# Optimization experiments

Hardware: AMD Instinct MI355X
Metric: run time of the kernel (lower is better)

The kernel has to match this reference:

```python
import jax, jax.numpy as jnp
import numpy as np


def setup_inputs() -> dict:
    key = jax.random.key(0)
    k1, k2, k3 = jax.random.split(key, 3)
    seq_len, input_size, hidden_size = 8192, 2048, 2048
    inputs = jax.random.normal(k1, (seq_len, input_size), dtype=jnp.float32)
    W_xh = jax.random.normal(k2, (hidden_size, input_size), dtype=jnp.float32) * 0.01
    W_hh = jax.random.normal(k3, (hidden_size, hidden_size), dtype=jnp.float32) * 0.01
    b_h = jnp.zeros((hidden_size, 1), dtype=jnp.float32)
    return {"inputs": inputs, "W_xh": W_xh, "W_hh": W_hh, "b_h": b_h}


def reference(inputs, W_xh, W_hh, b_h):
    # h_t = tanh(W_xh @ x_t + W_hh @ h_{t-1} + b_h), h_0 = 0
    # Torch code uses column vectors (hidden,1); we use flat (hidden,) vectors,
    # which is the same math.
    b = b_h[:, 0]
    h0 = jnp.zeros((W_hh.shape[0],), dtype=inputs.dtype)

    def step(h_prev, x_t):
        h_t = jnp.tanh(W_xh @ x_t + W_hh @ h_prev + b)
        return h_t, h_t

    h_T, outputs = jax.lax.scan(step, h0, inputs)
    # outputs: (seq_len, hidden)  == stacked list of h_t; h_T == final state
    return outputs, h_T
```

## Files before the change

### kernel.cpp

```cpp
#include <hip/hip_runtime.h>
#include <math.h>

#define H 2048
#define S 8192
#define RPB 16
#define NBLK (H / RPB)
#define PARBYTES (H * 4)
#define NREP 2

typedef unsigned int u32x4 __attribute__((ext_vector_type(4)));

__global__ __launch_bounds__(256) void gemm_xw(const float* __restrict__ X,
                                               const float* __restrict__ W,
                                               float* __restrict__ U) {
    __shared__ float As[16][64];
    __shared__ float Bs[16][64];
    const int tid = threadIdx.x;
    const int t0 = blockIdx.x * 64;
    const int j0 = blockIdx.y * 64;
    const int tx = tid & 15, ty = tid >> 4;

    float acc[4][4] = {};
    const int lr = tid >> 2;
    const int lk = (tid & 3) * 4;

    for (int k0 = 0; k0 < H; k0 += 16) {
        float4 a = *(const float4*)&X[(size_t)(t0 + lr) * H + k0 + lk];
        float4 b = *(const float4*)&W[(size_t)(j0 + lr) * H + k0 + lk];
        As[lk + 0][lr] = a.x; As[lk + 1][lr] = a.y; As[lk + 2][lr] = a.z; As[lk + 3][lr] = a.w;
        Bs[lk + 0][lr] = b.x; Bs[lk + 1][lr] = b.y; Bs[lk + 2][lr] = b.z; Bs[lk + 3][lr] = b.w;
        __syncthreads();
#pragma unroll
        for (int kk = 0; kk < 16; ++kk) {
            float4 av = *(const float4*)&As[kk][ty * 4];
            float4 bv = *(const float4*)&Bs[kk][tx * 4];
            float aa[4] = {av.x, av.y, av.z, av.w};
            float bb[4] = {bv.x, bv.y, bv.z, bv.w};
#pragma unroll
            for (int i = 0; i < 4; ++i)
#pragma unroll
                for (int j = 0; j < 4; ++j)
                    acc[i][j] += aa[i] * bb[j];
        }
        __syncthreads();
    }
#pragma unroll
    for (int i = 0; i < 4; ++i) {
        float4 v = {acc[i][0], acc[i][1], acc[i][2], acc[i][3]};
        *(float4*)&U[(size_t)(t0 + ty * 4 + i) * H + j0 + tx * 4] = v;
    }
}

__global__ void init_ws(unsigned long long* __restrict__ w) {
    int i = blockIdx.x * blockDim.x + threadIdx.x;
    if (i < NREP * 2 * (PARBYTES / 8))
        w[i] = ((i >> 10) & 1) ? 0x0000000100000001ull : 0ull;
}

__device__ inline void poll2(const void* pc, u32x4& c0, u32x4& c1) {
    asm volatile(
        "global_load_dwordx4 %0, %2, off sc1\n\t"
        "global_load_dwordx4 %1, %2, off offset:16 sc1\n\t"
        "s_waitcnt vmcnt(0)"
        : "=&v"(c0), "=&v"(c1)
        : "v"(pc)
        : "memory");
}
__device__ inline void st16_sc1(void* p, u32x4 v) {
    asm volatile("global_store_dwordx4 %0, %1, off sc1" :: "v"(p), "v"(v) : "memory");
}

__global__ __launch_bounds__(256) void rnn_recur(float* __restrict__ out,
                                                 const float* __restrict__ Whh,
                                                 const float* __restrict__ bias,
                                                 unsigned long long* __restrict__ hvt) {
    __shared__ float part[2][4][RPB];
    const int tid  = threadIdx.x;
    const int lane = tid & 63;
    const int wid  = tid >> 6;
    const int r0   = blockIdx.x * RPB;

    float4 wv[RPB][2];
#pragma unroll
    for (int j = 0; j < RPB; ++j)
#pragma unroll
        for (int i = 0; i < 2; ++i)
            wv[j][i] = *(const float4*)&Whh[(size_t)(r0 + j) * H + 8 * tid + 4 * i];

    const float bb = bias[r0 + (tid & 15)];
    char* const hrep = (char*)hvt + (size_t)(blockIdx.x & 1) * (2 * PARBYTES);

    for (int t = 0; t < S; ++t) {
        float u_val = out[(size_t)t * H + r0 + (tid & 15)];

        const unsigned int e  = ((unsigned int)t >> 1) & 3u;
        const unsigned int e0 = e & 1u, e1 = (e >> 1) & 1u;
        const char* pc = hrep + (size_t)(t & 1) * PARBYTES + tid * 32;

        float acc[RPB] = {};
        unsigned int pend = 3u;
        while (pend) {
            u32x4 c0, c1;
            poll2(pc, c0, c1);
#pragma unroll
            for (int i = 0; i < 2; ++i) {
                if (pend & (1u << i)) {
                    const u32x4 v = i ? c1 : c0;
                    if ((((v.x ^ e0) | (v.z ^ e0) | (v.y ^ e1) | (v.w ^ e1)) & 1u) == 0u) {
                        const float h0 = __uint_as_float(v.x), h1 = __uint_as_float(v.y);
                        const float h2 = __uint_as_float(v.z), h3 = __uint_as_float(v.w);
#pragma unroll
                        for (int j = 0; j < RPB; ++j)
                            acc[j] += wv[j][i].x * h0 + wv[j][i].y * h1 +
                                      wv[j][i].z * h2 + wv[j][i].w * h3;
                        pend &= ~(1u << i);
                    }
                }
            }
        }

#pragma unroll
        for (int j = 0; j < 8; ++j) {
            float s = (lane & 1) ? acc[j] : acc[j + 8];
            float r = __shfl_xor(s, 1, 64);
            acc[j] = ((lane & 1) ? acc[j + 8] : acc[j]) + r;
        }
#pragma unroll
        for (int j = 0; j < 4; ++j) {
            float s = (lane & 2) ? acc[j] : acc[j + 4];
            float r = __shfl_xor(s, 2, 64);
            acc[j] = ((lane & 2) ? acc[j + 4] : acc[j]) + r;
        }
#pragma unroll
        for (int j = 0; j < 2; ++j) {
            float s = (lane & 4) ? acc[j] : acc[j + 2];
            float r = __shfl_xor(s, 4, 64);
            acc[j] = ((lane & 4) ? acc[j + 2] : acc[j]) + r;
        }
        {
            float s = (lane & 8) ? acc[0] : acc[1];
            float r = __shfl_xor(s, 8, 64);
            acc[0] = ((lane & 8) ? acc[1] : acc[0]) + r;
        }
        acc[0] += __shfl_xor(acc[0], 16, 64);
        acc[0] += __shfl_xor(acc[0], 32, 64);

        if (lane < 16) {
            const int row = ((lane & 1) << 3) | ((lane & 2) << 1) |
                            ((lane & 4) >> 1) | ((lane & 8) >> 3);
            part[t & 1][wid][row] = acc[0];
        }
        __syncthreads();

        if (tid < RPB) {
            const float sum = part[t & 1][0][tid] + part[t & 1][1][tid] +
                              part[t & 1][2][tid] + part[t & 1][3][tid];
            const float val = tanhf(sum + u_val + bb);
            const float s0 = __shfl(val, (tid & 12) | 0, 64);
            const float s1 = __shfl(val, (tid & 12) | 1, 64);
            const float s2 = __shfl(val, (tid & 12) | 2, 64);
            const float s3 = __shfl(val, (tid & 12) | 3, 64);
            if ((tid & 3) == 0) {
                const unsigned int ee  = (((unsigned int)(t + 1)) >> 1) & 3u;
                const unsigned int ee0 = ee & 1u, ee1 = (ee >> 1) & 1u;
                u32x4 pk;
                pk.x = (__float_as_uint(s0) & ~1u) | ee0;
                pk.y = (__float_as_uint(s1) & ~1u) | ee1;
                pk.z = (__float_as_uint(s2) & ~1u) | ee0;
                pk.w = (__float_as_uint(s3) & ~1u) | ee1;
                char* dst = (char*)hvt + (size_t)((t + 1) & 1) * PARBYTES +
                            (size_t)(r0 + tid) * 4;
                asm volatile("s_waitcnt vmcnt(0)" ::: "memory");
#pragma unroll
                for (int rep = 0; rep < NREP; ++rep)
                    st16_sc1(dst + (size_t)rep * (2 * PARBYTES), pk);
            }
            out[(size_t)t * H + r0 + tid] = val;
            if (t == S - 1) out[(size_t)S * H + r0 + tid] = val;
        }
    }
}

extern "C" void kernel_launch(void* const* d_in, const int* in_sizes, int n_in,
                              void* d_out, int out_size, void* d_ws, size_t ws_size,
                              hipStream_t stream) {
    const float* X    = (const float*)d_in[0];
    const float* Wxh  = (const float*)d_in[1];
    const float* Whh  = (const float*)d_in[2];
    const float* bias = (const float*)d_in[3];
    float* out = (float*)d_out;
    unsigned long long* hvt = (unsigned long long*)d_ws;

    init_ws<<<(NREP * 2 * (PARBYTES / 8) + 255) / 256, 256, 0, stream>>>(hvt);

    dim3 ggrid(S / 64, H / 64);
    gemm_xw<<<ggrid, 256, 0, stream>>>(X, Wxh, out);

    void* args[] = {(void*)&out, (void*)&Whh, (void*)&bias, (void*)&hvt};
    hipLaunchCooperativeKernel((void*)rnn_recur, dim3(NBLK), dim3(256), args, 0, stream);
}
```

Before: 19.65 ms.

## Rebalance recurrent kernel to 64 blocks of 512 threads with 32 rows each

```diff
diff --git a/kernel.cpp b/kernel.cpp
--- a/kernel.cpp
+++ b/kernel.cpp
@@ -3,8 +3,9 @@
 
 #define H 2048
 #define S 8192
-#define RPB 16
+#define RPB 32
 #define NBLK (H / RPB)
+#define TPB 512
 #define PARBYTES (H * 4)
 #define NREP 2
 
@@ -57,109 +58,107 @@
         w[i] = ((i >> 10) & 1) ? 0x0000000100000001ull : 0ull;
 }
 
-__device__ inline void poll2(const void* pc, u32x4& c0, u32x4& c1) {
-    asm volatile(
-        "global_load_dwordx4 %0, %2, off sc1\n\t"
-        "global_load_dwordx4 %1, %2, off offset:16 sc1\n\t"
-        "s_waitcnt vmcnt(0)"
-        : "=&v"(c0), "=&v"(c1)
-        : "v"(pc)
-        : "memory");
+__device__ inline u32x4 ld16_sc1(const void* p) {
+    u32x4 r;
+    asm volatile("global_load_dwordx4 %0, %1, off sc1\n\t"
+                 "s_waitcnt vmcnt(0)"
+                 : "=&v"(r) : "v"(p) : "memory");
+    return r;
 }
 __device__ inline void st16_sc1(void* p, u32x4 v) {
     asm volatile("global_store_dwordx4 %0, %1, off sc1" :: "v"(p), "v"(v) : "memory");
 }
 
-__global__ __launch_bounds__(256) void rnn_recur(float* __restrict__ out,
-                                                 const float* __restrict__ Whh,
-                                                 const float* __restrict__ bias,
-                                                 unsigned long long* __restrict__ hvt) {
-    __shared__ float part[2][4][RPB];
+__global__ __launch_bounds__(TPB, 2) void rnn_recur(float* __restrict__ out,
+                                                    const float* __restrict__ Whh,
+                                                    const float* __restrict__ bias,
+                                                    unsigned long long* __restrict__ hvt) {
+    __shared__ float part[2][8][RPB];
     const int tid  = threadIdx.x;
     const int lane = tid & 63;
     const int wid  = tid >> 6;
     const int r0   = blockIdx.x * RPB;
 
-    float4 wv[RPB][2];
+    float4 wv[RPB];
 #pragma unroll
     for (int j = 0; j < RPB; ++j)
-#pragma unroll
-        for (int i = 0; i < 2; ++i)
-            wv[j][i] = *(const float4*)&Whh[(size_t)(r0 + j) * H + 8 * tid + 4 * i];
-
-    const float bb = bias[r0 + (tid & 15)];
+        wv[j] = *(const float4*)&Whh[(size_t)(r0 + j) * H + 4 * tid];
+
+    const float bb = bias[r0 + (tid & 31)];
     char* const hrep = (char*)hvt + (size_t)(blockIdx.x & 1) * (2 * PARBYTES);
 
     for (int t = 0; t < S; ++t) {
-        float u_val = out[(size_t)t * H + r0 + (tid & 15)];
+        float u_val = out[(size_t)t * H + r0 + (tid & 31)];
 
         const unsigned int e  = ((unsigned int)t >> 1) & 3u;
         const unsigned int e0 = e & 1u, e1 = (e >> 1) & 1u;
-        const char* pc = hrep + (size_t)(t & 1) * PARBYTES + tid * 32;
-
-        float acc[RPB] = {};
-        unsigned int pend = 3u;
+        const char* pc = hrep + (size_t)(t & 1) * PARBYTES + tid * 16;
+
+        float acc[RPB];
+#pragma unroll
+        for (int j = 0; j < RPB; ++j) acc[j] = 0.f;
+
+        unsigned int pend = 1u;
         while (pend) {
-            u32x4 c0, c1;
-            poll2(pc, c0, c1);
-#pragma unroll
-            for (int i = 0; i < 2; ++i) {
-                if (pend & (1u << i)) {
-                    const u32x4 v = i ? c1 : c0;
-                    if ((((v.x ^ e0) | (v.z ^ e0) | (v.y ^ e1) | (v.w ^ e1)) & 1u) == 0u) {
-                        const float h0 = __uint_as_float(v.x), h1 = __uint_as_float(v.y);
-                        const float h2 = __uint_as_float(v.z), h3 = __uint_as_float(v.w);
-#pragma unroll
-                        for (int j = 0; j < RPB; ++j)
-                            acc[j] += wv[j][i].x * h0 + wv[j][i].y * h1 +
-                                      wv[j][i].z * h2 + wv[j][i].w * h3;
-                        pend &= ~(1u << i);
-                    }
-                }
+            const u32x4 v = ld16_sc1(pc);
+            if ((((v.x ^ e0) | (v.z ^ e0) | (v.y ^ e1) | (v.w ^ e1)) & 1u) == 0u) {
+                const float h0 = __uint_as_float(v.x), h1 = __uint_as_float(v.y);
+                const float h2 = __uint_as_float(v.z), h3 = __uint_as_float(v.w);
+#pragma unroll
+                for (int j = 0; j < RPB; ++j)
+                    acc[j] += wv[j].x * h0 + wv[j].y * h1 +
+                              wv[j].z * h2 + wv[j].w * h3;
+                pend = 0u;
             }
         }
 
 #pragma unroll
+        for (int j = 0; j < 16; ++j) {
+            float s = (lane & 1) ? acc[j] : acc[j + 16];
+            float r = __shfl_xor(s, 1, 64);
+            acc[j] = ((lane & 1) ? acc[j + 16] : acc[j]) + r;
+        }
+#pragma unroll
         for (int j = 0; j < 8; ++j) {
-            float s = (lane & 1) ? acc[j] : acc[j + 8];
-            float r = __shfl_xor(s, 1, 64);
-            acc[j] = ((lane & 1) ? acc[j + 8] : acc[j]) + r;
+            float s = (lane & 2) ? acc[j] : acc[j + 8];
+            float r = __shfl_xor(s, 2, 64);
+            acc[j] = ((lane & 2) ? acc[j + 8] : acc[j]) + r;
         }
 #pragma unroll
         for (int j = 0; j < 4; ++j) {
-            float s = (lane & 2) ? acc[j] : acc[j + 4];
-            float r = __shfl_xor(s, 2, 64);
-            acc[j] = ((lane & 2) ? acc[j + 4] : acc[j]) + r;
+            float s = (lane & 4) ? acc[j] : acc[j + 4];
+            float r = __shfl_xor(s, 4, 64);
+            acc[j] = ((lane & 4) ? acc[j + 4] : acc[j]) + r;
         }
 #pragma unroll
         for (int j = 0; j < 2; ++j) {
-            float s = (lane & 4) ? acc[j] : acc[j + 2];
-            float r = __shfl_xor(s, 4, 64);
-            acc[j] = ((lane & 4) ? acc[j + 2] : acc[j]) + r;
+            float s = (lane & 8) ? acc[j] : acc[j + 2];
+            float r = __shfl_xor(s, 8, 64);
+            acc[j] = ((lane & 8) ? acc[j + 2] : acc[j]) + r;
         }
         {
-            float s = (lane & 8) ? acc[0] : acc[1];
-            float r = __shfl_xor(s, 8, 64);
-            acc[0] = ((lane & 8) ? acc[1] : acc[0]) + r;
-        }
-        acc[0] += __shfl_xor(acc[0], 16, 64);
+            float s = (lane & 16) ? acc[0] : acc[1];
+            float r = __shfl_xor(s, 16, 64);
+            acc[0] = ((lane & 16) ? acc[1] : acc[0]) + r;
+        }
         acc[0] += __shfl_xor(acc[0], 32, 64);
 
-        if (lane < 16) {
-            const int row = ((lane & 1) << 3) | ((lane & 2) << 1) |
-                            ((lane & 4) >> 1) | ((lane & 8) >> 3);
+        if (lane < 32) {
+            const int row = ((lane & 1) << 4) | ((lane & 2) << 2) | (lane & 4) |
+                            ((lane & 8) >> 2) | ((lane & 16) >> 4);
             part[t & 1][wid][row] = acc[0];
         }
         __syncthreads();
 
         if (tid < RPB) {
-            const float sum = part[t & 1][0][tid] + part[t & 1][1][tid] +
-                              part[t & 1][2][tid] + part[t & 1][3][tid];
+            float sum = 0.f;
+#pragma unroll
+            for (int w = 0; w < 8; ++w) sum += part[t & 1][w][tid];
             const float val = tanhf(sum + u_val + bb);
-            const float s0 = __shfl(val, (tid & 12) | 0, 64);
-            const float s1 = __shfl(val, (tid & 12) | 1, 64);
-            const float s2 = __shfl(val, (tid & 12) | 2, 64);
-            const float s3 = __shfl(val, (tid & 12) | 3, 64);
+            const float s0 = __shfl(val, (tid & 28) | 0, 64);
+            const float s1 = __shfl(val, (tid & 28) | 1, 64);
+            const float s2 = __shfl(val, (tid & 28) | 2, 64);
+            const float s3 = __shfl(val, (tid & 28) | 3, 64);
             if ((tid & 3) == 0) {
                 const unsigned int ee  = (((unsigned int)(t + 1)) >> 1) & 3u;
                 const unsigned int ee0 = ee & 1u, ee1 = (ee >> 1) & 1u;
@@ -197,5 +196,5 @@
     gemm_xw<<<ggrid, 256, 0, stream>>>(X, Wxh, out);
 
     void* args[] = {(void*)&out, (void*)&Whh, (void*)&bias, (void*)&hvt};
-    hipLaunchCooperativeKernel((void*)rnn_recur, dim3(NBLK), dim3(256), args, 0, stream);
-}
+    hipLaunchCooperativeKernel((void*)rnn_recur, dim3(NBLK), dim3(TPB), args, 0, stream);
+}
```

New measurement: 20.66 ms. 1.05x slower.
